# Optimization experiments

Measured on AMD Instinct MI355X. Metric: run time of the kernel, lower is better.

The kernel has to match this reference:

```python
import jax, jax.numpy as jnp
import numpy as np

DIM = 1024
N_HEADS = 16
HEAD_DIM = DIM // N_HEADS
MLP_RATIO = 4
LN_EPS = 1e-5


def _layer_norm(x, w):
    xf = x.astype(jnp.float32)
    mu = jnp.mean(xf, axis=-1, keepdims=True)
    var = jnp.var(xf, axis=-1, keepdims=True)
    y = (xf - mu) / jnp.sqrt(var + LN_EPS)
    return y * w[None, None, :]


def _apply_rope(x, cos, sin):
    # x: (b, s, h, d); cos, sin: (s, d/2)
    c = jnp.concatenate([cos, cos], axis=-1)[None, :, None, :]  # (1,s,1,d)
    s_ = jnp.concatenate([sin, sin], axis=-1)[None, :, None, :]
    x1, x2 = jnp.split(x, 2, axis=-1)
    rot = jnp.concatenate([-x2, x1], axis=-1)
    return x * c + rot * s_


def setup_inputs() -> dict:
    key = jax.random.key(0)
    ks = jax.random.split(key, 12)
    b, s = 2, 2048
    x = jax.random.normal(ks[0], (b, s, DIM), dtype=jnp.float32)
    rot_cos = jax.random.uniform(ks[1], (1, s, 1, 1, HEAD_DIM), dtype=jnp.float32)
    rot_sin = jax.random.uniform(ks[2], (1, s, 1, 1, HEAD_DIM), dtype=jnp.float32)
    w_init = 0.02
    params = {
        'ln1_w': jnp.ones((DIM,), jnp.float32),
        'w_qkv': jax.random.normal(ks[3], (3 * DIM, DIM), jnp.float32) * w_init,
        'w_out': jax.random.normal(ks[4], (DIM, DIM), jnp.float32) * w_init,
        'ln2_w': jnp.ones((DIM,), jnp.float32),
        'w_mlp1': jax.random.normal(ks[5], (MLP_RATIO * DIM, DIM), jnp.float32) * w_init,
        'b_mlp1': jnp.zeros((MLP_RATIO * DIM,), jnp.float32),
        'w_mlp2': jax.random.normal(ks[6], (DIM, MLP_RATIO * DIM), jnp.float32) * w_init,
        'b_mlp2': jnp.zeros((DIM,), jnp.float32),
    }
    return {'x': x, 'rot_cos': rot_cos, 'rot_sin': rot_sin, **params}


def reference(x, rot_cos, rot_sin, ln1_w, w_qkv, w_out, ln2_w, w_mlp1, b_mlp1, w_mlp2, b_mlp2):
    b, s, _ = x.shape
    # _split_rotary: (1,s,1,1,hd) -> (s, hd/2)
    cos = rot_cos[0, :, 0, 0, : HEAD_DIM // 2]
    sin = rot_sin[0, :, 0, 0, : HEAD_DIM // 2]

    x_skip = x
    h1 = _layer_norm(x, ln1_w)
    qkv = jnp.einsum('bsd,ed->bse', h1, w_qkv).reshape(b, s, 3, N_HEADS, HEAD_DIM)
    q, k, v = qkv[:, :, 0], qkv[:, :, 1], qkv[:, :, 2]
    q = _apply_rope(q, cos, sin)
    k = _apply_rope(k, cos, sin)

    # causal SDPA, scale = 1/sqrt(head_dim) (flex_attention default)
    scale = 1.0 / np.sqrt(HEAD_DIM)
    scores = jnp.einsum('bqhd,bkhd->bhqk', q, k) * scale
    causal = jnp.tril(jnp.ones((s, s), dtype=bool))
    scores = jnp.where(causal[None, None], scores, -jnp.inf)
    attn = jax.nn.softmax(scores, axis=-1)
    o = jnp.einsum('bhqk,bkhd->bqhd', attn, v).reshape(b, s, DIM)

    # attn out + residual (eval: dropout off, scale=1)
    x = x_skip + jnp.einsum('bsd,ed->bse', o, w_out)

    # MLP with tanh GELU + residual
    h2 = _layer_norm(x, ln2_w)
    u = jnp.einsum('bsd,ed->bse', h2, w_mlp1) + b_mlp1
    u = jax.nn.gelu(u, approximate=True)
    m = jnp.einsum('bse,de->bsd', u, w_mlp2) + b_mlp2
    return x + m
```

## Files before the change

### kernel.cpp

```cpp
#include <hip/hip_runtime.h>
#include <hip/hip_bf16.h>
#include <math.h>


#define B_ 2
#define S_ 2048
#define D_ 1024
#define H_ 16
#define DH_ 64
#define MLP_ 4096
#define ROWS_ (B_ * S_)

typedef short bf16x8 __attribute__((ext_vector_type(8)));
typedef float f32x4 __attribute__((ext_vector_type(4)));
typedef unsigned short ushort_t;
typedef ushort_t u16x4 __attribute__((ext_vector_type(4)));
typedef unsigned int u32x2 __attribute__((ext_vector_type(2)));

__device__ __forceinline__ float wave_reduce_sum(float v) {
  #pragma unroll
  for (int off = 32; off > 0; off >>= 1) v += __shfl_down(v, off, 64);
  return v;
}

__device__ __forceinline__ ushort_t f2bf(float v) {
  __hip_bfloat16 h = __float2bfloat16(v);
  return *(ushort_t*)&h;
}
__device__ __forceinline__ float bf2f(ushort_t u) {
  unsigned int v = ((unsigned int)u) << 16;
  union { unsigned int i; float f; } c; c.i = v; return c.f;
}

__device__ __forceinline__ void async_copy16(const void* g, void* l) {
  __builtin_amdgcn_global_load_lds(
      (const __attribute__((address_space(1))) void*)g,
      (__attribute__((address_space(3))) void*)l, 16, 0, 0);
}

__global__ __launch_bounds__(256) void cast_w_kernel(
    const float* __restrict__ s0, ushort_t* __restrict__ d0, int n0,
    const float* __restrict__ s1, ushort_t* __restrict__ d1, int n1,
    const float* __restrict__ s2, ushort_t* __restrict__ d2, int n2,
    const float* __restrict__ s3, ushort_t* __restrict__ d3, int n3) {
  const float* s; ushort_t* d; int n;
  switch (blockIdx.y) {
    case 0: s = s0; d = d0; n = n0; break;
    case 1: s = s1; d = d1; n = n1; break;
    case 2: s = s2; d = d2; n = n2; break;
    default: s = s3; d = d3; n = n3; break;
  }
  const int i = (blockIdx.x * 256 + threadIdx.x) * 4;
  if (i < n) {
    const float4 v = *reinterpret_cast<const float4*>(s + i);
    u16x4 o;
    o[0] = f2bf(v.x); o[1] = f2bf(v.y); o[2] = f2bf(v.z); o[3] = f2bf(v.w);
    *reinterpret_cast<u16x4*>(d + i) = o;
  }
}

__global__ __launch_bounds__(256) void ln_kernel(
    const float* __restrict__ x, const float* __restrict__ w,
    ushort_t* __restrict__ y) {
  const int row = blockIdx.x;
  const float4 v = reinterpret_cast<const float4*>(x + (size_t)row * D_)[threadIdx.x];
  float s  = v.x + v.y + v.z + v.w;
  float ss = v.x * v.x + v.y * v.y + v.z * v.z + v.w * v.w;
  __shared__ float red[8];
  const int wave = threadIdx.x >> 6, lane = threadIdx.x & 63;
  const float ws1 = wave_reduce_sum(s);
  const float ws2 = wave_reduce_sum(ss);
  if (lane == 0) { red[wave] = ws1; red[4 + wave] = ws2; }
  __syncthreads();
  const float tot  = red[0] + red[1] + red[2] + red[3];
  const float tot2 = red[4] + red[5] + red[6] + red[7];
  const float mu  = tot * (1.0f / D_);
  const float var = tot2 * (1.0f / D_) - mu * mu;
  const float inv = rsqrtf(var + 1e-5f);
  const float4 wv = reinterpret_cast<const float4*>(w)[threadIdx.x];
  u16x4 o;
  o[0] = f2bf((v.x - mu) * inv * wv.x);
  o[1] = f2bf((v.y - mu) * inv * wv.y);
  o[2] = f2bf((v.z - mu) * inv * wv.z);
  o[3] = f2bf((v.w - mu) * inv * wv.w);
  reinterpret_cast<u16x4*>(y + (size_t)row * D_)[threadIdx.x] = o;
}

__device__ __forceinline__ float gelu_tanh(float u) {
  const float u3 = u * u * u;
  const float t = tanhf(0.7978845608028654f * (u + 0.044715f * u3));
  return 0.5f * u * (1.0f + t);
}

template <int FUSE, int OUTBF, int QKV>
__global__ __launch_bounds__(256) void gemm_bt(
    const ushort_t* __restrict__ A, const ushort_t* __restrict__ W,
    const float* __restrict__ bias, const float* __restrict__ res,
    void* __restrict__ Cv, ushort_t* __restrict__ VtOut,
    int M, int N, int K, int sm, int sn, int rects_n) {
  __shared__ ushort_t As[2][128 * 32];
  __shared__ ushort_t Bs[2][128 * 32];
  const int tid = threadIdx.x;
  const int wave = tid >> 6, lane = tid & 63;
  const int l15 = lane & 15, quad = lane >> 4;

  const int lin = blockIdx.x;
  const int xcd = lin & 7, j = lin >> 3;
  const int rm = xcd / rects_n, rn = xcd % rects_n;
  const int m0 = (rm * sm + (j % sm)) * 128;
  const int n0 = (rn * sn + (j / sm)) * 128;
  const int wm = (wave & 1) * 64, wn = (wave >> 1) * 64;

  const int srow = tid >> 2;
  const int gcol = (((tid & 3) ^ (srow & 3)) * 8);
  const ushort_t* Ag = A + (size_t)(m0 + srow) * K + gcol;
  const ushort_t* Wg = W + (size_t)(n0 + srow) * K + gcol;

  f32x4 acc[4][4] = {};
  const int rslot = (quad ^ (l15 & 3)) * 8;

  const int NI = K >> 5;
  async_copy16(Ag,          &As[0][tid * 8]);
  async_copy16(Ag + 64 * K, &As[0][2048 + tid * 8]);
  async_copy16(Wg,          &Bs[0][tid * 8]);
  async_copy16(Wg + 64 * K, &Bs[0][2048 + tid * 8]);

  for (int i = 0; i < NI; ++i) {
    const int st = i & 1;
    __syncthreads();
    if (i + 1 < NI) {
      const int k1 = (i + 1) << 5;
      async_copy16(Ag + k1,          &As[1 - st][tid * 8]);
      async_copy16(Ag + 64 * K + k1, &As[1 - st][2048 + tid * 8]);
      async_copy16(Wg + k1,          &Bs[1 - st][tid * 8]);
      async_copy16(Wg + 64 * K + k1, &Bs[1 - st][2048 + tid * 8]);
    }
    bf16x8 af[4], bfr[4];
    #pragma unroll
    for (int ii = 0; ii < 4; ++ii) {
      af[ii]  = *(const bf16x8*)&As[st][(wm + ii * 16 + l15) * 32 + rslot];
      bfr[ii] = *(const bf16x8*)&Bs[st][(wn + ii * 16 + l15) * 32 + rslot];
    }
    #pragma unroll
    for (int ii = 0; ii < 4; ++ii)
      #pragma unroll
      for (int jj = 0; jj < 4; ++jj)
        acc[ii][jj] = __builtin_amdgcn_mfma_f32_16x16x32_bf16(af[ii], bfr[jj], acc[ii][jj], 0, 0, 0);
  }

  #pragma unroll
  for (int i = 0; i < 4; ++i) {
    const int mb = m0 + wm + i * 16 + quad * 4;
    #pragma unroll
    for (int jj = 0; jj < 4; ++jj) {
      const int n = n0 + wn + jj * 16 + l15;
      float cv[4];
      #pragma unroll
      for (int r = 0; r < 4; ++r) {
        float c = acc[i][jj][r];
        if (FUSE & 1) c += bias[n];
        if (FUSE & 2) c = gelu_tanh(c);
        if (FUSE & 4) c += res[(size_t)(mb + r) * N + n];
        cv[r] = c;
      }
      if (QKV && ((n0 + wn) >> 10) == 2) {
        const int d  = n & 63;
        const int hh = (n >> 6) & 15;
        const int bb = mb >> 11;
        const int ss = mb & (S_ - 1);
        u16x4 pk;
        #pragma unroll
        for (int r = 0; r < 4; ++r) pk[r] = f2bf(cv[r]);
        *(u16x4*)&VtOut[((size_t)(bb * H_ + hh) * DH_ + d) * S_ + ss] = pk;
      } else {
        #pragma unroll
        for (int r = 0; r < 4; ++r) {
          if (OUTBF) ((ushort_t*)Cv)[(size_t)(mb + r) * N + n] = f2bf(cv[r]);
          else       ((float*)Cv)[(size_t)(mb + r) * N + n]   = cv[r];
        }
      }
    }
  }
}

template <int FUSE, int OUTBF>
__global__ __launch_bounds__(256) void gemm64_bt(
    const ushort_t* __restrict__ A, const ushort_t* __restrict__ W,
    const float* __restrict__ bias, const float* __restrict__ res,
    void* __restrict__ Cv, int M, int N, int K, int sm, int sn, int rects_n) {
  __shared__ ushort_t As[2][64 * 64];
  __shared__ ushort_t Bs[2][128 * 64];
  const int tid = threadIdx.x;
  const int wave = tid >> 6, lane = tid & 63;
  const int l15 = lane & 15, quad = lane >> 4;

  const int lin = blockIdx.x;
  const int xcd = lin & 7, j = lin >> 3;
  const int rm = xcd / rects_n, rn = xcd % rects_n;
  const int m0 = (rm * sm + (j % sm)) * 64;
  const int n0 = (rn * sn + (j / sm)) * 128;
  const int wn = wave * 32;

  const int srow = tid >> 3;
  const int gcol = (((tid & 7) ^ (srow & 7)) * 8);
  const ushort_t* Ag = A + (size_t)(m0 + srow) * K + gcol;
  const ushort_t* Wg = W + (size_t)(n0 + srow) * K + gcol;

  f32x4 acc[4][2] = {};

  const int NI = K >> 6;
  #pragma unroll
  for (int i = 0; i < 2; ++i)
    async_copy16(Ag + (size_t)i * 32 * K, &As[0][i * 2048 + tid * 8]);
  #pragma unroll
  for (int i = 0; i < 4; ++i)
    async_copy16(Wg + (size_t)i * 32 * K, &Bs[0][i * 2048 + tid * 8]);

  for (int it = 0; it < NI; ++it) {
    const int st = it & 1;
    __syncthreads();
    if (it + 1 < NI) {
      const int k1 = (it + 1) << 6;
      #pragma unroll
      for (int i = 0; i < 2; ++i)
        async_copy16(Ag + (size_t)i * 32 * K + k1, &As[1 - st][i * 2048 + tid * 8]);
      #pragma unroll
      for (int i = 0; i < 4; ++i)
        async_copy16(Wg + (size_t)i * 32 * K + k1, &Bs[1 - st][i * 2048 + tid * 8]);
    }
    #pragma unroll
    for (int kk = 0; kk < 2; ++kk) {
      const int slot = (((kk * 4 + quad) ^ (l15 & 7)) * 8);
      bf16x8 af[4], bfr[2];
      #pragma unroll
      for (int i = 0; i < 4; ++i)
        af[i] = *(const bf16x8*)&As[st][(i * 16 + l15) * 64 + slot];
      #pragma unroll
      for (int jj = 0; jj < 2; ++jj)
        bfr[jj] = *(const bf16x8*)&Bs[st][(wn + jj * 16 + l15) * 64 + slot];
      #pragma unroll
      for (int i = 0; i < 4; ++i)
        #pragma unroll
        for (int jj = 0; jj < 2; ++jj)
          acc[i][jj] = __builtin_amdgcn_mfma_f32_16x16x32_bf16(af[i], bfr[jj], acc[i][jj], 0, 0, 0);
    }
  }

  #pragma unroll
  for (int i = 0; i < 4; ++i) {
    const int mb = m0 + i * 16 + quad * 4;
    #pragma unroll
    for (int jj = 0; jj < 2; ++jj) {
      const int n = n0 + wn + jj * 16 + l15;
      #pragma unroll
      for (int r = 0; r < 4; ++r) {
        float c = acc[i][jj][r];
        if (FUSE & 1) c += bias[n];
        if (FUSE & 2) c = gelu_tanh(c);
        if (FUSE & 4) c += res[(size_t)(mb + r) * N + n];
        if (OUTBF) ((ushort_t*)Cv)[(size_t)(mb + r) * N + n] = f2bf(c);
        else       ((float*)Cv)[(size_t)(mb + r) * N + n]   = c;
      }
    }
  }
}

__global__ __launch_bounds__(256) void rope_kernel(
    const ushort_t* __restrict__ qkv, const float* __restrict__ cosb,
    const float* __restrict__ sinb, ushort_t* __restrict__ Qo,
    ushort_t* __restrict__ Ko) {
  const int bs = blockIdx.x;
  const int s  = bs & (S_ - 1);
  const int b  = bs >> 11;
  const int t  = threadIdx.x;
  const ushort_t* base = qkv + (size_t)bs * (3 * D_);
  #pragma unroll
  for (int i = 0; i < 8; ++i) {
    const int e = i * 256 + t;
    const int which = e >> 10;
    const int rem = e & 1023;
    const int h = rem >> 6;
    const int d = rem & 63;
    const float val = bf2f(base[e]);
    float out;
    if (d < 32) {
      out = val * cosb[s * 64 + d] - bf2f(base[e + 32]) * sinb[s * 64 + d];
    } else {
      out = val * cosb[s * 64 + d - 32] + bf2f(base[e - 32]) * sinb[s * 64 + d - 32];
    }
    const size_t oidx = (((size_t)(b * H_ + h)) * S_ + s) * DH_ + d;
    if (which == 0) Qo[oidx] = f2bf(out * 0.125f);
    else            Ko[oidx] = f2bf(out);
  }
}

#define PPAD 72

__global__ __launch_bounds__(256) void attn_kernel(
    const ushort_t* __restrict__ Qb, const ushort_t* __restrict__ Kb,
    const ushort_t* __restrict__ Vt, ushort_t* __restrict__ O) {
  const int wave = threadIdx.x >> 6;
  const int lane = threadIdx.x & 63;
  const int l15 = lane & 15, quad = lane >> 4;
  const int bh = blockIdx.y;
  const int b = bh >> 4, h = bh & 15;
  const int wl = blockIdx.x * 4 + wave;
  const int g  = (wl & 1) ? (63 - (wl >> 1)) : (wl >> 1);
  const int q0 = g * 32;

  __shared__ ushort_t Plds[4][2][16 * PPAD];

  const ushort_t* Kbh = Kb + (size_t)bh * S_ * DH_;
  const ushort_t* Vbh = Vt + (size_t)bh * DH_ * S_;

  bf16x8 qb[2][2];
  #pragma unroll
  for (int t = 0; t < 2; ++t) {
    const ushort_t* qptr = Qb + ((size_t)bh * S_ + q0 + t * 16 + l15) * DH_ + quad * 8;
    qb[t][0] = *(const bf16x8*)(qptr);
    qb[t][1] = *(const bf16x8*)(qptr + 32);
  }

  f32x4 o_acc[2][4] = {};
  float m_run[2] = {-1e30f, -1e30f}, l_run[2] = {0.0f, 0.0f};

  const int nch = (q0 >> 6) + 1;

  bf16x8 ka[4][2];
  #pragma unroll
  for (int kt = 0; kt < 4; ++kt) {
    const ushort_t* kp = Kbh + (size_t)(kt * 16 + l15) * DH_ + quad * 8;
    ka[kt][0] = *(const bf16x8*)kp;
    ka[kt][1] = *(const bf16x8*)(kp + 32);
  }

  for (int c = 0; c < nch; ++c) {
    const int k0 = c << 6;

    bf16x8 va[4][2];
    #pragma unroll
    for (int mt = 0; mt < 4; ++mt) {
      const ushort_t* vp = Vbh + (size_t)(mt * 16 + l15) * S_ + k0 + quad * 8;
      va[mt][0] = *(const bf16x8*)vp;
      va[mt][1] = *(const bf16x8*)(vp + 32);
    }

    f32x4 st[2][4];
    #pragma unroll
    for (int t = 0; t < 2; ++t)
      #pragma unroll
      for (int kt = 0; kt < 4; ++kt) {
        f32x4 z = {0.0f, 0.0f, 0.0f, 0.0f};
        z = __builtin_amdgcn_mfma_f32_16x16x32_bf16(ka[kt][0], qb[t][0], z, 0, 0, 0);
        z = __builtin_amdgcn_mfma_f32_16x16x32_bf16(ka[kt][1], qb[t][1], z, 0, 0, 0);
        st[t][kt] = z;
      }

    if (c + 1 < nch) {
      const int k1 = (c + 1) << 6;
      bf16x8 kan[4][2];
      #pragma unroll
      for (int kt = 0; kt < 4; ++kt) {
        const ushort_t* kp = Kbh + (size_t)(k1 + kt * 16 + l15) * DH_ + quad * 8;
        kan[kt][0] = *(const bf16x8*)kp;
        kan[kt][1] = *(const bf16x8*)(kp + 32);
      }
      #pragma unroll
      for (int kt = 0; kt < 4; ++kt) { ka[kt][0] = kan[kt][0]; ka[kt][1] = kan[kt][1]; }
    }

    if (c == nch - 1) {
      #pragma unroll
      for (int t = 0; t < 2; ++t) {
        const int query = q0 + t * 16 + l15;
        #pragma unroll
        for (int kt = 0; kt < 4; ++kt)
          #pragma unroll
          for (int r = 0; r < 4; ++r)
            if (k0 + kt * 16 + quad * 4 + r > query) st[t][kt][r] = -1e30f;
      }
    }

    #pragma unroll
    for (int t = 0; t < 2; ++t) {
      float mx = -1e30f;
      #pragma unroll
      for (int kt = 0; kt < 4; ++kt)
        #pragma unroll
        for (int r = 0; r < 4; ++r) mx = fmaxf(mx, st[t][kt][r]);
      mx = fmaxf(mx, __shfl_xor(mx, 16, 64));
      mx = fmaxf(mx, __shfl_xor(mx, 32, 64));
      const float m_new = fmaxf(m_run[t], mx);
      const float alpha = __expf(m_run[t] - m_new);
      float rs = 0.0f;
      #pragma unroll
      for (int kt = 0; kt < 4; ++kt)
        #pragma unroll
        for (int r = 0; r < 4; ++r) {
          const float e = __expf(st[t][kt][r] - m_new);
          st[t][kt][r] = e;
          rs += e;
        }
      rs += __shfl_xor(rs, 16, 64);
      rs += __shfl_xor(rs, 32, 64);
      l_run[t] = l_run[t] * alpha + rs;
      m_run[t] = m_new;
      #pragma unroll
      for (int mt = 0; mt < 4; ++mt)
        #pragma unroll
        for (int r = 0; r < 4; ++r) o_acc[t][mt][r] *= alpha;
    }

    #pragma unroll
    for (int t = 0; t < 2; ++t) {
      ushort_t* Pw = &Plds[wave][t][0];
      #pragma unroll
      for (int kt = 0; kt < 4; ++kt) {
        u32x2 wpair;
        wpair[0] = (unsigned)f2bf(st[t][kt][0]) | ((unsigned)f2bf(st[t][kt][1]) << 16);
        wpair[1] = (unsigned)f2bf(st[t][kt][2]) | ((unsigned)f2bf(st[t][kt][3]) << 16);
        *(u32x2*)&Pw[l15 * PPAD + kt * 16 + quad * 4] = wpair;
      }
      asm volatile("s_waitcnt lgkmcnt(0)" ::: "memory");
      const bf16x8 pb0 = *(const bf16x8*)&Pw[l15 * PPAD + quad * 8];
      const bf16x8 pb1 = *(const bf16x8*)&Pw[l15 * PPAD + 32 + quad * 8];
      #pragma unroll
      for (int mt = 0; mt < 4; ++mt) {
        o_acc[t][mt] = __builtin_amdgcn_mfma_f32_16x16x32_bf16(va[mt][0], pb0, o_acc[t][mt], 0, 0, 0);
        o_acc[t][mt] = __builtin_amdgcn_mfma_f32_16x16x32_bf16(va[mt][1], pb1, o_acc[t][mt], 0, 0, 0);
      }
    }
  }

  #pragma unroll
  for (int t = 0; t < 2; ++t) {
    const float inv = 1.0f / l_run[t];
    #pragma unroll
    for (int mt = 0; mt < 4; ++mt) {
      u16x4 pk;
      #pragma unroll
      for (int r = 0; r < 4; ++r) pk[r] = f2bf(o_acc[t][mt][r] * inv);
      *(u16x4*)&O[(((size_t)b * S_ + q0 + t * 16 + l15) * H_ + h) * DH_ + mt * 16 + quad * 4] = pk;
    }
  }
}

extern "C" void kernel_launch(void* const* d_in, const int* in_sizes, int n_in,
                              void* d_out, int out_size, void* d_ws, size_t ws_size,
                              hipStream_t stream) {
  const float* x       = (const float*)d_in[0];
  const float* rot_cos = (const float*)d_in[1];
  const float* rot_sin = (const float*)d_in[2];
  const float* ln1_w   = (const float*)d_in[3];
  const float* w_qkv   = (const float*)d_in[4];
  const float* w_out   = (const float*)d_in[5];
  const float* ln2_w   = (const float*)d_in[6];
  const float* w_mlp1  = (const float*)d_in[7];
  const float* b_mlp1  = (const float*)d_in[8];
  const float* w_mlp2  = (const float*)d_in[9];
  const float* b_mlp2  = (const float*)d_in[10];
  float* out = (float*)d_out;

  char* wsb = (char*)d_ws;
  const size_t MB = 1u << 20;
  ushort_t* h1_bf  = (ushort_t*)(wsb + 0 * MB);
  ushort_t* qkv_bf = (ushort_t*)(wsb + 8 * MB);
  ushort_t* q_bf   = (ushort_t*)(wsb + 32 * MB);
  ushort_t* k_bf   = (ushort_t*)(wsb + 40 * MB);
  ushort_t* v_t    = (ushort_t*)(wsb + 48 * MB);
  ushort_t* o_bf   = (ushort_t*)(wsb + 56 * MB);
  float*    x2     = (float*)   (wsb + 64 * MB);
  ushort_t* u_bf   = (ushort_t*)(wsb + 80 * MB);
  ushort_t* wq_bf  = (ushort_t*)(wsb + 112 * MB);
  ushort_t* wo_bf  = (ushort_t*)(wsb + 118 * MB);
  ushort_t* w1_bf  = (ushort_t*)(wsb + 120 * MB);
  ushort_t* w2_bf  = (ushort_t*)(wsb + 128 * MB);
  (void)ws_size; (void)in_sizes; (void)n_in; (void)out_size;

  dim3 b256(256);

  cast_w_kernel<<<dim3(4096, 4), b256, 0, stream>>>(
      w_qkv, wq_bf, 3 * D_ * D_, w_out, wo_bf, D_ * D_,
      w_mlp1, w1_bf, MLP_ * D_, w_mlp2, w2_bf, MLP_ * D_);
  ln_kernel<<<dim3(ROWS_), b256, 0, stream>>>(x, ln1_w, h1_bf);
  gemm_bt<0, 1, 1><<<dim3(768), b256, 0, stream>>>(
      h1_bf, wq_bf, nullptr, nullptr, qkv_bf, v_t, ROWS_, 3 * D_, D_, 16, 6, 4);
  rope_kernel<<<dim3(ROWS_), b256, 0, stream>>>(qkv_bf, rot_cos, rot_sin, q_bf, k_bf);
  attn_kernel<<<dim3(16, B_ * H_), b256, 0, stream>>>(q_bf, k_bf, v_t, o_bf);
  gemm64_bt<4, 0><<<dim3(512), b256, 0, stream>>>(
      o_bf, wo_bf, nullptr, x, x2, ROWS_, D_, D_, 16, 4, 2);
  ln_kernel<<<dim3(ROWS_), b256, 0, stream>>>(x2, ln2_w, h1_bf);
  gemm_bt<3, 1, 0><<<dim3(1024), b256, 0, stream>>>(
      h1_bf, w1_bf, b_mlp1, nullptr, u_bf, nullptr, ROWS_, MLP_, D_, 16, 8, 4);
  gemm64_bt<5, 0><<<dim3(512), b256, 0, stream>>>(
      u_bf, w2_bf, b_mlp2, x2, out, ROWS_, D_, MLP_, 16, 4, 2);
}
```

Measured before the change: 388.1 us.

## Split attention KV chunks across wave pairs with LDS softmax merge, XCD-aware mapping

Each 32-query tile is now processed by two waves that take alternating 64-key chunks, and their partial softmax states are merged through shared memory at the end. The grid becomes 1024 linear blocks mapped so that blocks of the same head land on the same XCD, with short and long causal tiles paired in one block. The softmax switches to exp2 by folding log2(e) into the Q scale. The intent is to double wave-level parallelism and shorten the per-wave critical path, at the cost of a block-wide sync, extra LDS, and a merge step.

```diff
diff --git a/kernel.cpp b/kernel.cpp
--- a/kernel.cpp
+++ b/kernel.cpp
@@ -289,7 +289,7 @@
       out = val * cosb[s * 64 + d - 32] + bf2f(base[e - 32]) * sinb[s * 64 + d - 32];
     }
     const size_t oidx = (((size_t)(b * H_ + h)) * S_ + s) * DH_ + d;
-    if (which == 0) Qo[oidx] = f2bf(out * 0.125f);
+    if (which == 0) Qo[oidx] = f2bf(out * 0.18033688f);
     else            Ko[oidx] = f2bf(out);
   }
 }
@@ -302,13 +302,18 @@
   const int wave = threadIdx.x >> 6;
   const int lane = threadIdx.x & 63;
   const int l15 = lane & 15, quad = lane >> 4;
-  const int bh = blockIdx.y;
+  const int lin = blockIdx.x;
+  const int xcd = lin & 7;
+  const int k = lin >> 3;
+  const int bh = xcd + 8 * (k & 3);
+  const int xb = k >> 2;
   const int b = bh >> 4, h = bh & 15;
-  const int wl = blockIdx.x * 4 + wave;
-  const int g  = (wl & 1) ? (63 - (wl >> 1)) : (wl >> 1);
+  const int g = (wave < 2) ? xb : (63 - xb);
+  const int par = wave & 1;
   const int q0 = g * 32;
 
   __shared__ ushort_t Plds[4][2][16 * PPAD];
+  __shared__ float Comb[2][64][36];
 
   const ushort_t* Kbh = Kb + (size_t)bh * S_ * DH_;
   const ushort_t* Vbh = Vt + (size_t)bh * DH_ * S_;
@@ -329,12 +334,12 @@
   bf16x8 ka[4][2];
   #pragma unroll
   for (int kt = 0; kt < 4; ++kt) {
-    const ushort_t* kp = Kbh + (size_t)(kt * 16 + l15) * DH_ + quad * 8;
+    const ushort_t* kp = Kbh + (size_t)(par * 64 + kt * 16 + l15) * DH_ + quad * 8;
     ka[kt][0] = *(const bf16x8*)kp;
     ka[kt][1] = *(const bf16x8*)(kp + 32);
   }
 
-  for (int c = 0; c < nch; ++c) {
+  for (int c = par; c < nch; c += 2) {
     const int k0 = c << 6;
 
     bf16x8 va[4][2];
@@ -356,8 +361,8 @@
         st[t][kt] = z;
       }
 
-    if (c + 1 < nch) {
-      const int k1 = (c + 1) << 6;
+    if (c + 2 < nch) {
+      const int k1 = (c + 2) << 6;
       bf16x8 kan[4][2];
       #pragma unroll
       for (int kt = 0; kt < 4; ++kt) {
@@ -391,13 +396,13 @@
       mx = fmaxf(mx, __shfl_xor(mx, 16, 64));
       mx = fmaxf(mx, __shfl_xor(mx, 32, 64));
       const float m_new = fmaxf(m_run[t], mx);
-      const float alpha = __expf(m_run[t] - m_new);
+      const float alpha = exp2f(m_run[t] - m_new);
       float rs = 0.0f;
       #pragma unroll
       for (int kt = 0; kt < 4; ++kt)
         #pragma unroll
         for (int r = 0; r < 4; ++r) {
-          const float e = __expf(st[t][kt][r] - m_new);
+          const float e = exp2f(st[t][kt][r] - m_new);
           st[t][kt][r] = e;
           rs += e;
         }
@@ -432,15 +437,38 @@
     }
   }
 
-  #pragma unroll
-  for (int t = 0; t < 2; ++t) {
-    const float inv = 1.0f / l_run[t];
-    #pragma unroll
-    for (int mt = 0; mt < 4; ++mt) {
-      u16x4 pk;
-      #pragma unroll
-      for (int r = 0; r < 4; ++r) pk[r] = f2bf(o_acc[t][mt][r] * inv);
-      *(u16x4*)&O[(((size_t)b * S_ + q0 + t * 16 + l15) * H_ + h) * DH_ + mt * 16 + quad * 4] = pk;
+  if (par == 1) {
+    float* dst = &Comb[wave >> 1][lane][0];
+    dst[0] = m_run[0]; dst[1] = l_run[0];
+    dst[2] = m_run[1]; dst[3] = l_run[1];
+    #pragma unroll
+    for (int t = 0; t < 2; ++t)
+      #pragma unroll
+      for (int mt = 0; mt < 4; ++mt)
+        #pragma unroll
+        for (int r = 0; r < 4; ++r)
+          dst[4 + t * 16 + mt * 4 + r] = o_acc[t][mt][r];
+  }
+  __syncthreads();
+  if (par == 0) {
+    const float* src = &Comb[wave >> 1][lane][0];
+    #pragma unroll
+    for (int t = 0; t < 2; ++t) {
+      const float mB = src[t * 2], lB = src[t * 2 + 1];
+      const float m_new = fmaxf(m_run[t], mB);
+      const float aA = exp2f(m_run[t] - m_new);
+      const float aB = exp2f(mB - m_new);
+      const float inv = 1.0f / (l_run[t] * aA + lB * aB);
+      #pragma unroll
+      for (int mt = 0; mt < 4; ++mt) {
+        u16x4 pk;
+        #pragma unroll
+        for (int r = 0; r < 4; ++r) {
+          const float o = o_acc[t][mt][r] * aA + src[4 + t * 16 + mt * 4 + r] * aB;
+          pk[r] = f2bf(o * inv);
+        }
+        *(u16x4*)&O[(((size_t)b * S_ + q0 + t * 16 + l15) * H_ + h) * DH_ + mt * 16 + quad * 4] = pk;
+      }
     }
   }
 }
@@ -486,7 +514,7 @@
   gemm_bt<0, 1, 1><<<dim3(768), b256, 0, stream>>>(
       h1_bf, wq_bf, nullptr, nullptr, qkv_bf, v_t, ROWS_, 3 * D_, D_, 16, 6, 4);
   rope_kernel<<<dim3(ROWS_), b256, 0, stream>>>(qkv_bf, rot_cos, rot_sin, q_bf, k_bf);
-  attn_kernel<<<dim3(16, B_ * H_), b256, 0, stream>>>(q_bf, k_bf, v_t, o_bf);
+  attn_kernel<<<dim3(1024), b256, 0, stream>>>(q_bf, k_bf, v_t, o_bf);
   gemm64_bt<4, 0><<<dim3(512), b256, 0, stream>>>(
       o_bf, wo_bf, nullptr, x, x2, ROWS_, D_, D_, 16, 4, 2);
   ln_kernel<<<dim3(ROWS_), b256, 0, stream>>>(x2, ln2_w, h1_bf);
```

New measurement: 389.0 us. Within noise of the previous version (+0.2%).
